# Kernel optimization log

Measured on AMD Instinct MI355X. Metric: run time of the kernel, lower is better.

The kernel has to match this reference:

```python
import jax, jax.numpy as jnp
import numpy as np

LAYER_NUMBER = 1  # coeff for query_key_layer_scaling; cancels mathematically
HEAD_DIM = 128

def setup_inputs() -> dict:
    key = jax.random.key(0)
    k1, k2, k3, k4 = jax.random.split(key, 4)
    s, b, h, d = 2048, 2, 16, HEAD_DIM
    return {
        "query_layer": jax.random.normal(k1, (s, b, h, d), dtype=jnp.float32),
        "key_layer": jax.random.normal(k2, (s, b, h, d), dtype=jnp.float32),
        "value_layer": jax.random.normal(k3, (s, b, h, d), dtype=jnp.float32),
        "attention_mask": jax.random.randint(k4, (b, 1, s, s), 0, 2).astype(jnp.bool_),
    }

def reference(query_layer, key_layer, value_layer, attention_mask):
    s, b, h, d = query_layer.shape
    # norm_factor = sqrt(d) * layer_number; softmax scale (coeff) = layer_number
    norm_factor = jnp.sqrt(jnp.asarray(d, jnp.float32)) * LAYER_NUMBER
    coeff = jnp.asarray(LAYER_NUMBER, jnp.float32)
    # raw scores [b, h, sq, sk]
    scores = jnp.einsum('sbhd,tbhd->bhst', query_layer, key_layer) / norm_factor
    # fused scale-mask-softmax, in fp32 (attention_softmax_in_fp32=True)
    scores32 = scores.astype(jnp.float32) * coeff
    scores32 = jnp.where(attention_mask, jnp.float32(-10000.0), scores32)
    probs = jax.nn.softmax(scores32, axis=-1).astype(query_layer.dtype)
    # dropout p=0.0 -> identity
    # context: [b, h, sq, d] -> [sq, b, h*d]
    ctx = jnp.einsum('bhst,tbhd->sbhd', probs, value_layer)
    return ctx.reshape(s, b, h * d)
```

## Files before the change

### kernel.cpp

```cpp
#include <hip/hip_runtime.h>
#include <hip/hip_bf16.h>

#define S_LEN 2048
#define NB 2
#define NH 16
#define DH 128
#define ROW_STRIDE (NB * NH * DH)
#define M_TILE 128
#define N_TILE 64
#define NKT (S_LEN / N_TILE)
#define NWORDS (NB * S_LEN * (S_LEN / 64))

typedef __bf16 bf16x8_t __attribute__((ext_vector_type(8)));
typedef __bf16 bf16x4_t __attribute__((ext_vector_type(4)));
typedef float  f32x4_t  __attribute__((ext_vector_type(4)));

#define AS1 __attribute__((address_space(1)))
#define AS3 __attribute__((address_space(3)))

__device__ __forceinline__ void gload_lds16(const void* g, void* l) {
    __builtin_amdgcn_global_load_lds((const AS1 void*)g, (AS3 void*)l, 16, 0, 0);
}

__device__ __forceinline__ float vexp2(float x) {
    float r;
    asm("v_exp_f32 %0, %1" : "=v"(r) : "v"(x));
    return r;
}
__device__ __forceinline__ unsigned vcvtpk(float a, float b) {
    unsigned r;
    asm("v_cvt_pk_bf16_f32 %0, %1, %2" : "=v"(r) : "v"(a), "v"(b));
    return r;
}

template <int CTRL>
__device__ __forceinline__ float dppmov(float x) {
    return __builtin_bit_cast(float,
        __builtin_amdgcn_update_dpp(0, __builtin_bit_cast(int, x), CTRL, 0xF, 0xF, true));
}
__device__ __forceinline__ float rowmax16(float x) {
    x = fmaxf(x, dppmov<0xB1>(x));
    x = fmaxf(x, dppmov<0x4E>(x));
    x = fmaxf(x, dppmov<0x141>(x));
    x = fmaxf(x, dppmov<0x140>(x));
    return x;
}
__device__ __forceinline__ float rowsum16(float x) {
    x += dppmov<0xB1>(x);
    x += dppmov<0x4E>(x);
    x += dppmov<0x141>(x);
    x += dppmov<0x140>(x);
    return x;
}

__global__ __launch_bounds__(256) void prep_kernel(
    const float* __restrict__ Kg, const float* __restrict__ Vg,
    const int* __restrict__ Mg,
    __bf16* __restrict__ Kb, __bf16* __restrict__ Vb,
    unsigned long long* __restrict__ Wg)
{
    __shared__ float tf[64][129];
    const int tid = threadIdx.x;
    const int blk = blockIdx.x;

    if (blk < 4096) {
        const int idx = blk * 256 + tid;
        const int d8 = (idx & 15) * 8;
        const int t  = (idx >> 4) & (S_LEN - 1);
        const int bh = idx >> 15;
        const int b = bh >> 4, h = bh & (NH - 1);
        const float* src = Kg + (size_t)t * ROW_STRIDE + b * (NH * DH) + h * DH + d8;
        float4 f0 = *(const float4*)src;
        float4 f1 = *(const float4*)(src + 4);
        bf16x8_t v;
        v[0] = (__bf16)f0.x; v[1] = (__bf16)f0.y; v[2] = (__bf16)f0.z; v[3] = (__bf16)f0.w;
        v[4] = (__bf16)f1.x; v[5] = (__bf16)f1.y; v[6] = (__bf16)f1.z; v[7] = (__bf16)f1.w;
        *(bf16x8_t*)(Kb + ((size_t)bh * S_LEN + t) * DH + d8) = v;
    } else if (blk < 5120) {
        const int vb = blk - 4096;
        const int bh = vb >> 5;
        const int tc = vb & 31;
        const int b = bh >> 4, h = bh & (NH - 1);
        const int t0 = tc * 64;
        const int head_off = b * (NH * DH) + h * DH;
#pragma unroll
        for (int i = 0; i < 8; ++i) {
            int idx = i * 256 + tid;
            int t  = idx >> 5;
            int d4 = (idx & 31) * 4;
            float4 f = *(const float4*)(Vg + (size_t)(t0 + t) * ROW_STRIDE + head_off + d4);
            tf[t][d4 + 0] = f.x; tf[t][d4 + 1] = f.y;
            tf[t][d4 + 2] = f.z; tf[t][d4 + 3] = f.w;
        }
        __syncthreads();
#pragma unroll
        for (int i = 0; i < 8; ++i) {
            int idx = i * 256 + tid;
            int d  = idx >> 4;
            int t4 = (idx & 15) * 4;
            bf16x4_t w;
            w[0] = (__bf16)tf[t4 + 0][d];
            w[1] = (__bf16)tf[t4 + 1][d];
            w[2] = (__bf16)tf[t4 + 2][d];
            w[3] = (__bf16)tf[t4 + 3][d];
            *(bf16x4_t*)(Vb + ((size_t)bh * DH + d) * S_LEN + t0 + t4) = w;
        }
    } else {
        const int lane = tid & 63;
        const int wv = ((blk - 5120) * 256 + tid) >> 6;
#pragma unroll
        for (int i = 0; i < 16; ++i) {
            const int wid = wv * 16 + i;
            const int v = Mg[(size_t)wid * 64 + lane];
            const unsigned long long bal = __ballot(v != 0);
            if (lane == 0) Wg[wid] = bal;
        }
    }
}

__global__ __launch_bounds__(256) void mask_pack(
    const int* __restrict__ Mg, unsigned long long* __restrict__ Wg)
{
    const int lane = threadIdx.x & 63;
    const int wv = (blockIdx.x * blockDim.x + threadIdx.x) >> 6;
#pragma unroll
    for (int i = 0; i < 4; ++i) {
        const int wid = wv * 4 + i;
        const int v = Mg[(size_t)wid * 64 + lane];
        const unsigned long long bal = __ballot(v != 0);
        if (lane == 0) Wg[wid] = bal;
    }
}

__global__ __launch_bounds__(256, 2) void fa_kernel(
    const float* __restrict__ Qg, const __bf16* __restrict__ Kb,
    const __bf16* __restrict__ Vb, const unsigned long long* __restrict__ Mw,
    float* __restrict__ Og)
{
    __shared__ __bf16 kT[2][64 * 128];
    __shared__ __bf16 vT[2][128 * 64];

    const int tid  = threadIdx.x;
    const int wave = tid >> 6;
    const int lane = tid & 63;
    const int l15  = lane & 15;
    const int quad = lane >> 4;
    const int swz  = (l15 & 7) << 4;

    const int bid = blockIdx.x;
    const int lb  = ((bid & 7) << 6) | (bid >> 3);
    const int qt  = lb & 15;
    const int bh  = lb >> 4;
    const int h   = bh & (NH - 1);
    const int b   = bh >> 4;

    const int q0       = qt * M_TILE;
    const int head_off = b * (NH * DH) + h * DH;

    const float kScale = 1.44269504088896340736f / 11.31370849898476039f;

    const uint2* mrow = (const uint2*)Mw
        + (size_t)b * (S_LEN * (S_LEN / 64))
        + (size_t)(q0 + wave * 32) * (S_LEN / 64);

    const char* KbBH = (const char*)(Kb + (size_t)bh * S_LEN * DH);
    const char* VbBH = (const char*)(Vb + (size_t)bh * DH * S_LEN);

    int kOff[4], vOff[4];
#pragma unroll
    for (int i = 0; i < 4; ++i) {
        const int chunk = (wave * 4 + i) * 64 + lane;
        const int tr = chunk >> 4;
        const int ck = chunk & 15;
        kOff[i] = tr * 256 + ((ck * 16) ^ ((tr & 7) << 4));
        const int dv = chunk >> 3;
        const int cv = chunk & 7;
        vOff[i] = dv * (S_LEN * 2) + ((cv * 16) ^ ((dv & 7) << 4));
    }

    bf16x8_t qf[2][4];
#pragma unroll
    for (int mt = 0; mt < 2; ++mt) {
        const int srow = q0 + wave * 32 + mt * 16 + l15;
        const float* qp = Qg + (size_t)srow * ROW_STRIDE + head_off + quad * 8;
#pragma unroll
        for (int kc = 0; kc < 4; ++kc) {
            float4 f0 = *(const float4*)(qp + kc * 32);
            float4 f1 = *(const float4*)(qp + kc * 32 + 4);
            bf16x8_t v;
            v[0] = (__bf16)(f0.x * kScale); v[1] = (__bf16)(f0.y * kScale);
            v[2] = (__bf16)(f0.z * kScale); v[3] = (__bf16)(f0.w * kScale);
            v[4] = (__bf16)(f1.x * kScale); v[5] = (__bf16)(f1.y * kScale);
            v[6] = (__bf16)(f1.z * kScale); v[7] = (__bf16)(f1.w * kScale);
            qf[mt][kc] = v;
        }
    }

    f32x4_t oacc[2][8];
    float lsum[2];
#pragma unroll
    for (int mt = 0; mt < 2; ++mt) {
#pragma unroll
        for (int dt = 0; dt < 8; ++dt) oacc[mt][dt] = {0.0f, 0.0f, 0.0f, 0.0f};
        lsum[mt] = 0.0f;
    }

    auto STAGE = [&](int buf, int kt_) {
        const char* ks = KbBH + (size_t)kt_ * (N_TILE * DH * 2);
        const char* vs = VbBH + (size_t)kt_ * (N_TILE * 2);
#pragma unroll
        for (int i = 0; i < 4; ++i)
            gload_lds16(ks + kOff[i], (char*)&kT[buf][0] + (wave * 4 + i) * 1024);
#pragma unroll
        for (int i = 0; i < 4; ++i)
            gload_lds16(vs + vOff[i], (char*)&vT[buf][0] + (wave * 4 + i) * 1024);
    };

    STAGE(0, 0);
    asm volatile("s_waitcnt vmcnt(0)" ::: "memory");
    __builtin_amdgcn_s_barrier();
    int cur = 0;

    for (int kt = 0; kt < NKT; ++kt) {
        if (kt + 1 < NKT) STAGE(cur ^ 1, kt + 1);

        uint2 mwv[2];
#pragma unroll
        for (int mt = 0; mt < 2; ++mt)
            mwv[mt] = mrow[(size_t)(mt * 16 + l15) * (S_LEN / 64) + kt];

        const char* kbuf = (const char*)&kT[cur][0];
        f32x4_t sacc[2][4];
#pragma unroll
        for (int mt = 0; mt < 2; ++mt)
#pragma unroll
            for (int n = 0; n < 4; ++n) sacc[mt][n] = {0.0f, 0.0f, 0.0f, 0.0f};
        __builtin_amdgcn_s_setprio(1);
#pragma unroll
        for (int n = 0; n < 4; ++n) {
#pragma unroll
            for (int kc = 0; kc < 4; ++kc) {
                bf16x8_t kb = *(const bf16x8_t*)(kbuf + (n * 16 + l15) * 256
                                                 + ((kc * 64 + quad * 16) ^ swz));
                sacc[0][n] = __builtin_amdgcn_mfma_f32_16x16x32_bf16(kb, qf[0][kc], sacc[0][n], 0, 0, 0);
                sacc[1][n] = __builtin_amdgcn_mfma_f32_16x16x32_bf16(kb, qf[1][kc], sacc[1][n], 0, 0, 0);
            }
        }
        __builtin_amdgcn_s_setprio(0);

        unsigned pk[2][4][2];
#pragma unroll
        for (int mt = 0; mt < 2; ++mt) {
            const unsigned ex0 = mwv[mt].x >> (quad * 4);
            const unsigned ex1 = mwv[mt].y >> (quad * 4);
            float p[4][4];
#pragma unroll
            for (int n = 0; n < 4; ++n) {
                const unsigned ex = (n < 2) ? ex0 : ex1;
                const int sh = (n & 1) * 16;
#pragma unroll
                for (int r = 0; r < 4; ++r) {
                    const float e = vexp2(sacc[mt][n][r]);
                    p[n][r] = ((ex >> (sh + r)) & 1u) ? 0.0f : e;
                }
            }
            float s01 = (p[0][0] + p[0][1]) + (p[0][2] + p[0][3]);
            float s11 = (p[1][0] + p[1][1]) + (p[1][2] + p[1][3]);
            float s21 = (p[2][0] + p[2][1]) + (p[2][2] + p[2][3]);
            float s31 = (p[3][0] + p[3][1]) + (p[3][2] + p[3][3]);
            lsum[mt] += (s01 + s11) + (s21 + s31);
#pragma unroll
            for (int n = 0; n < 4; ++n) {
                pk[mt][n][0] = vcvtpk(p[n][0], p[n][1]);
                pk[mt][n][1] = vcvtpk(p[n][2], p[n][3]);
            }
        }

        const char* vbuf = (const char*)&vT[cur][0];
        __builtin_amdgcn_s_setprio(1);
#pragma unroll
        for (int kc2 = 0; kc2 < 2; ++kc2) {
            bf16x8_t af[2];
#pragma unroll
            for (int mt = 0; mt < 2; ++mt) {
                int4 a;
                a.x = (int)pk[mt][2 * kc2][0];
                a.y = (int)pk[mt][2 * kc2][1];
                a.z = (int)pk[mt][2 * kc2 + 1][0];
                a.w = (int)pk[mt][2 * kc2 + 1][1];
                af[mt] = __builtin_bit_cast(bf16x8_t, a);
            }
#pragma unroll
            for (int dt = 0; dt < 8; ++dt) {
                const char* vrow = vbuf + (dt * 16 + l15) * 128;
                bf16x4_t v0 = *(const bf16x4_t*)(vrow + ((kc2 * 64 + quad * 8) ^ swz));
                bf16x4_t v1 = *(const bf16x4_t*)(vrow + ((kc2 * 64 + quad * 8 + 32) ^ swz));
                bf16x8_t bfr = __builtin_shufflevector(v0, v1, 0, 1, 2, 3, 4, 5, 6, 7);
                oacc[0][dt] = __builtin_amdgcn_mfma_f32_16x16x32_bf16(af[0], bfr, oacc[0][dt], 0, 0, 0);
                oacc[1][dt] = __builtin_amdgcn_mfma_f32_16x16x32_bf16(af[1], bfr, oacc[1][dt], 0, 0, 0);
            }
        }
        __builtin_amdgcn_s_setprio(0);

        asm volatile("s_waitcnt vmcnt(0)" ::: "memory");
        __builtin_amdgcn_s_barrier();
        cur ^= 1;
    }

#pragma unroll
    for (int mt = 0; mt < 2; ++mt) {
        float tot = lsum[mt];
        tot += __shfl_xor(tot, 16, 64);
        tot += __shfl_xor(tot, 32, 64);
#pragma unroll
        for (int r = 0; r < 4; ++r) {
            const float inv = 1.0f / __shfl(tot, quad * 4 + r, 64);
            const int srow = q0 + wave * 32 + mt * 16 + quad * 4 + r;
            float* op = Og + (size_t)srow * ROW_STRIDE + head_off + l15;
#pragma unroll
            for (int dt = 0; dt < 8; ++dt) op[dt * 16] = oacc[mt][dt][r] * inv;
        }
    }
}

#define LDS_KS 136
#define LDS_VS 72
#define LDS_PS 68

__global__ __launch_bounds__(256, 2) void fa_kernel_fb(
    const float* __restrict__ Qg, const float* __restrict__ Kg,
    const float* __restrict__ Vg, const unsigned long long* __restrict__ Mw,
    float* __restrict__ Og)
{
    __shared__ __bf16 kT[64 * LDS_KS];
    __shared__ __bf16 vT[DH * LDS_VS];
    __shared__ __bf16 pT[4 * 32 * LDS_PS];

    const int tid  = threadIdx.x;
    const int wave = tid >> 6;
    const int lane = tid & 63;
    const int l15  = lane & 15;
    const int quad = lane >> 4;

    const int bid = blockIdx.x;
    const int qt  = bid & 15;
    const int bh  = bid >> 4;
    const int h   = bh & (NH - 1);
    const int b   = bh >> 4;

    const int q0       = qt * M_TILE;
    const int head_off = b * (NH * DH) + h * DH;

    const float kScale   = 1.44269504088896340736f / 11.31370849898476039f;
    const float kMaskVal = -14426.950408889634f;
    const float kThr     = 8.0f;

    const uint2* mrow = (const uint2*)Mw
        + (size_t)b * (S_LEN * (S_LEN / 64))
        + (size_t)(q0 + wave * 32) * (S_LEN / 64);

    bf16x8_t qf[2][4];
#pragma unroll
    for (int mt = 0; mt < 2; ++mt) {
        const int srow = q0 + wave * 32 + mt * 16 + l15;
        const float* qp = Qg + (size_t)srow * ROW_STRIDE + head_off + quad * 8;
#pragma unroll
        for (int kc = 0; kc < 4; ++kc) {
            float4 f0 = *(const float4*)(qp + kc * 32);
            float4 f1 = *(const float4*)(qp + kc * 32 + 4);
            bf16x8_t v;
            v[0] = (__bf16)f0.x; v[1] = (__bf16)f0.y;
            v[2] = (__bf16)f0.z; v[3] = (__bf16)f0.w;
            v[4] = (__bf16)f1.x; v[5] = (__bf16)f1.y;
            v[6] = (__bf16)f1.z; v[7] = (__bf16)f1.w;
            qf[mt][kc] = v;
        }
    }

    f32x4_t oacc[2][8];
    float mstate[2][4], lstate[2][4];
#pragma unroll
    for (int mt = 0; mt < 2; ++mt) {
#pragma unroll
        for (int dt = 0; dt < 8; ++dt) oacc[mt][dt] = {0.0f, 0.0f, 0.0f, 0.0f};
#pragma unroll
        for (int r = 0; r < 4; ++r) { mstate[mt][r] = -3.0e38f; lstate[mt][r] = 0.0f; }
    }

    __bf16* pW = &pT[wave * 32 * LDS_PS];

    for (int kt = 0; kt < NKT; ++kt) {
        const int t0 = kt * N_TILE;
        __syncthreads();

        {
            const int r0 = tid >> 5;
            const int c4 = (tid & 31) * 4;
            const float* kp = Kg + (size_t)(t0 + r0) * ROW_STRIDE + head_off + c4;
            __bf16* kd = &kT[r0 * LDS_KS + c4];
#pragma unroll
            for (int rr = 0; rr < 8; ++rr) {
                float4 f = *(const float4*)kp;
                bf16x4_t w;
                w[0] = (__bf16)f.x; w[1] = (__bf16)f.y;
                w[2] = (__bf16)f.z; w[3] = (__bf16)f.w;
                *(bf16x4_t*)kd = w;
                kp += 8 * ROW_STRIDE;
                kd += 8 * LDS_KS;
            }
        }
        {
            const int dv = tid & 31;
            const int tg = tid >> 5;
            const float* vbase = Vg + (size_t)(t0 + tg * 8) * ROW_STRIDE + head_off + dv;
#pragma unroll
            for (int j = 0; j < 4; ++j) {
                const int d = dv + j * 32;
#pragma unroll
                for (int tt = 0; tt < 2; ++tt) {
                    const float* vp = vbase + j * 32 + (size_t)(tt * 4) * ROW_STRIDE;
                    bf16x4_t w;
                    w[0] = (__bf16)vp[0 * ROW_STRIDE];
                    w[1] = (__bf16)vp[1 * ROW_STRIDE];
                    w[2] = (__bf16)vp[2 * ROW_STRIDE];
                    w[3] = (__bf16)vp[3 * ROW_STRIDE];
                    *(bf16x4_t*)&vT[d * LDS_VS + tg * 8 + tt * 4] = w;
                }
            }
        }
        __syncthreads();

        uint2 mw[2][4];
#pragma unroll
        for (int mt = 0; mt < 2; ++mt)
#pragma unroll
            for (int r = 0; r < 4; ++r)
                mw[mt][r] = mrow[(size_t)(mt * 16 + quad * 4 + r) * (S_LEN / 64) + kt];

        f32x4_t sacc[2][4];
#pragma unroll
        for (int mt = 0; mt < 2; ++mt)
#pragma unroll
            for (int n = 0; n < 4; ++n) sacc[mt][n] = {0.0f, 0.0f, 0.0f, 0.0f};
#pragma unroll
        for (int n = 0; n < 4; ++n) {
#pragma unroll
            for (int kc = 0; kc < 4; ++kc) {
                bf16x8_t kb = *(const bf16x8_t*)&kT[(n * 16 + l15) * LDS_KS + kc * 32 + quad * 8];
                sacc[0][n] = __builtin_amdgcn_mfma_f32_16x16x32_bf16(qf[0][kc], kb, sacc[0][n], 0, 0, 0);
                sacc[1][n] = __builtin_amdgcn_mfma_f32_16x16x32_bf16(qf[1][kc], kb, sacc[1][n], 0, 0, 0);
            }
        }

#pragma unroll
        for (int mt = 0; mt < 2; ++mt) {
            float sv[4][4];
            float tmv[4];
#pragma unroll
            for (int r = 0; r < 4; ++r) {
                const unsigned a0 = mw[mt][r].x >> l15;
                const unsigned a1 = mw[mt][r].y >> l15;
                sv[0][r] = (a0 & 1u)       ? kMaskVal : sacc[mt][0][r] * kScale;
                sv[1][r] = (a0 & 0x10000u) ? kMaskVal : sacc[mt][1][r] * kScale;
                sv[2][r] = (a1 & 1u)       ? kMaskVal : sacc[mt][2][r] * kScale;
                sv[3][r] = (a1 & 0x10000u) ? kMaskVal : sacc[mt][3][r] * kScale;
                float tm = fmaxf(fmaxf(sv[0][r], sv[1][r]), fmaxf(sv[2][r], sv[3][r]));
                tmv[r] = rowmax16(tm);
            }
            bool need = (tmv[0] > mstate[mt][0] + kThr) |
                        (tmv[1] > mstate[mt][1] + kThr) |
                        (tmv[2] > mstate[mt][2] + kThr) |
                        (tmv[3] > mstate[mt][3] + kThr);
            if (__any(need)) {
#pragma unroll
                for (int r = 0; r < 4; ++r) {
                    const float mold  = mstate[mt][r];
                    const float mnew  = fmaxf(mold, tmv[r]);
                    const float alpha = vexp2(mold - mnew);
                    float rsum = 0.0f;
#pragma unroll
                    for (int n = 0; n < 4; ++n) {
                        float p = vexp2(sv[n][r] - mnew);
                        rsum += p;
                        pW[(mt * 16 + quad * 4 + r) * LDS_PS + n * 16 + l15] = (__bf16)p;
                    }
                    rsum = rowsum16(rsum);
                    lstate[mt][r] = lstate[mt][r] * alpha + rsum;
                    mstate[mt][r] = mnew;
#pragma unroll
                    for (int dt = 0; dt < 8; ++dt) oacc[mt][dt][r] *= alpha;
                }
            } else {
#pragma unroll
                for (int r = 0; r < 4; ++r) {
                    const float mold = mstate[mt][r];
                    float rsum = 0.0f;
#pragma unroll
                    for (int n = 0; n < 4; ++n) {
                        float p = vexp2(sv[n][r] - mold);
                        rsum += p;
                        pW[(mt * 16 + quad * 4 + r) * LDS_PS + n * 16 + l15] = (__bf16)p;
                    }
                    lstate[mt][r] += rowsum16(rsum);
                }
            }
        }

#pragma unroll
        for (int kc2 = 0; kc2 < 2; ++kc2) {
            bf16x8_t af[2];
#pragma unroll
            for (int mt = 0; mt < 2; ++mt) {
                bf16x4_t lo = *(const bf16x4_t*)&pW[(mt * 16 + l15) * LDS_PS + kc2 * 32 + quad * 8];
                bf16x4_t hi = *(const bf16x4_t*)&pW[(mt * 16 + l15) * LDS_PS + kc2 * 32 + quad * 8 + 4];
                af[mt] = __builtin_shufflevector(lo, hi, 0, 1, 2, 3, 4, 5, 6, 7);
            }
#pragma unroll
            for (int dt = 0; dt < 8; ++dt) {
                bf16x8_t bfr = *(const bf16x8_t*)&vT[(dt * 16 + l15) * LDS_VS + kc2 * 32 + quad * 8];
                oacc[0][dt] = __builtin_amdgcn_mfma_f32_16x16x32_bf16(af[0], bfr, oacc[0][dt], 0, 0, 0);
                oacc[1][dt] = __builtin_amdgcn_mfma_f32_16x16x32_bf16(af[1], bfr, oacc[1][dt], 0, 0, 0);
            }
        }
    }

#pragma unroll
    for (int mt = 0; mt < 2; ++mt) {
#pragma unroll
        for (int r = 0; r < 4; ++r) {
            const float inv = 1.0f / lstate[mt][r];
            const int srow = q0 + wave * 32 + mt * 16 + quad * 4 + r;
            float* op = Og + (size_t)srow * ROW_STRIDE + head_off + l15;
#pragma unroll
            for (int dt = 0; dt < 8; ++dt) op[dt * 16] = oacc[mt][dt][r] * inv;
        }
    }
}

extern "C" void kernel_launch(void* const* d_in, const int* in_sizes, int n_in,
                              void* d_out, int out_size, void* d_ws, size_t ws_size,
                              hipStream_t stream) {
    (void)in_sizes; (void)n_in; (void)out_size;
    const float* Q = (const float*)d_in[0];
    const float* K = (const float*)d_in[1];
    const float* V = (const float*)d_in[2];
    const int*   M = (const int*)d_in[3];
    float* O = (float*)d_out;

    const size_t need_fast = ((size_t)33 << 20);

    if (ws_size >= need_fast) {
        __bf16* Kb = (__bf16*)d_ws;
        __bf16* Vb = (__bf16*)((char*)d_ws + ((size_t)16 << 20));
        unsigned long long* Mw = (unsigned long long*)((char*)d_ws + ((size_t)32 << 20));
        hipLaunchKernelGGL(prep_kernel, dim3(7168), dim3(256), 0, stream, K, V, M, Kb, Vb, Mw);
        hipLaunchKernelGGL(fa_kernel, dim3(NB * NH * (S_LEN / M_TILE)), dim3(256), 0, stream,
                           Q, Kb, Vb, Mw, O);
    } else {
        unsigned long long* Mw = (unsigned long long*)d_ws;
        hipLaunchKernelGGL(mask_pack, dim3(NWORDS / 4 * 64 / 256), dim3(256), 0, stream, M, Mw);
        hipLaunchKernelGGL(fa_kernel_fb, dim3(NB * NH * (S_LEN / M_TILE)), dim3(256), 0, stream,
                           Q, K, V, Mw, O);
    }
}
```

Baseline: 259.7 us.

## Pre-swizzle K/V tiles in prep and use 8 waves of 16 query rows

The prep kernel now writes K and V as contiguous pre-swizzled 16KB bf16 tiles in exactly the LDS layout, so the attention kernel stages each tile with plain linear global-to-LDS copies and reads V fragments as single 16-byte loads instead of two 8-byte loads. The attention kernel moves from 4 waves handling 32 query rows each to 8 waves (512 threads) handling 16 rows each, halving per-wave accumulator registers to raise occupancy. The trade-off is fewer MFMAs per K/V LDS fragment load, since each K and V fragment now feeds one query tile instead of two, which raises LDS traffic per unit of work.

```diff
diff --git a/kernel.cpp b/kernel.cpp
--- a/kernel.cpp
+++ b/kernel.cpp
@@ -63,32 +63,38 @@
     const int tid = threadIdx.x;
     const int blk = blockIdx.x;
 
-    if (blk < 4096) {
-        const int idx = blk * 256 + tid;
-        const int d8 = (idx & 15) * 8;
-        const int t  = (idx >> 4) & (S_LEN - 1);
-        const int bh = idx >> 15;
+    if (blk < 1024) {
+        const int bh = blk >> 5;
+        const int kt = blk & 31;
         const int b = bh >> 4, h = bh & (NH - 1);
-        const float* src = Kg + (size_t)t * ROW_STRIDE + b * (NH * DH) + h * DH + d8;
-        float4 f0 = *(const float4*)src;
-        float4 f1 = *(const float4*)(src + 4);
-        bf16x8_t v;
-        v[0] = (__bf16)f0.x; v[1] = (__bf16)f0.y; v[2] = (__bf16)f0.z; v[3] = (__bf16)f0.w;
-        v[4] = (__bf16)f1.x; v[5] = (__bf16)f1.y; v[6] = (__bf16)f1.z; v[7] = (__bf16)f1.w;
-        *(bf16x8_t*)(Kb + ((size_t)bh * S_LEN + t) * DH + d8) = v;
-    } else if (blk < 5120) {
-        const int vb = blk - 4096;
+        const int head_off = b * (NH * DH) + h * DH;
+        char* tile = (char*)Kb + (size_t)blk * 16384;
+#pragma unroll
+        for (int it = 0; it < 4; ++it) {
+            const int idx = it * 256 + tid;
+            const int tl = idx >> 4;
+            const int d8 = (idx & 15) * 8;
+            const float* src = Kg + (size_t)(kt * 64 + tl) * ROW_STRIDE + head_off + d8;
+            float4 f0 = *(const float4*)src;
+            float4 f1 = *(const float4*)(src + 4);
+            bf16x8_t v;
+            v[0] = (__bf16)f0.x; v[1] = (__bf16)f0.y; v[2] = (__bf16)f0.z; v[3] = (__bf16)f0.w;
+            v[4] = (__bf16)f1.x; v[5] = (__bf16)f1.y; v[6] = (__bf16)f1.z; v[7] = (__bf16)f1.w;
+            *(bf16x8_t*)(tile + tl * 256 + ((d8 * 2) ^ ((tl & 7) << 4))) = v;
+        }
+    } else if (blk < 2048) {
+        const int vb = blk - 1024;
         const int bh = vb >> 5;
-        const int tc = vb & 31;
+        const int kt = vb & 31;
         const int b = bh >> 4, h = bh & (NH - 1);
-        const int t0 = tc * 64;
         const int head_off = b * (NH * DH) + h * DH;
+        char* tile = (char*)Vb + (size_t)vb * 16384;
 #pragma unroll
         for (int i = 0; i < 8; ++i) {
             int idx = i * 256 + tid;
             int t  = idx >> 5;
             int d4 = (idx & 31) * 4;
-            float4 f = *(const float4*)(Vg + (size_t)(t0 + t) * ROW_STRIDE + head_off + d4);
+            float4 f = *(const float4*)(Vg + (size_t)(kt * 64 + t) * ROW_STRIDE + head_off + d4);
             tf[t][d4 + 0] = f.x; tf[t][d4 + 1] = f.y;
             tf[t][d4 + 2] = f.z; tf[t][d4 + 3] = f.w;
         }
@@ -103,11 +109,12 @@
             w[1] = (__bf16)tf[t4 + 1][d];
             w[2] = (__bf16)tf[t4 + 2][d];
             w[3] = (__bf16)tf[t4 + 3][d];
-            *(bf16x4_t*)(Vb + ((size_t)bh * DH + d) * S_LEN + t0 + t4) = w;
+            const int col = (t4 & 32) * 2 + ((t4 >> 2) & 3) * 16 + ((t4 & 16) >> 1);
+            *(bf16x4_t*)(tile + d * 128 + (col ^ ((d & 7) << 4))) = w;
         }
     } else {
         const int lane = tid & 63;
-        const int wv = ((blk - 5120) * 256 + tid) >> 6;
+        const int wv = ((blk - 2048) * 256 + tid) >> 6;
 #pragma unroll
         for (int i = 0; i < 16; ++i) {
             const int wid = wv * 16 + i;
@@ -132,7 +139,7 @@
     }
 }
 
-__global__ __launch_bounds__(256, 2) void fa_kernel(
+__global__ __launch_bounds__(512, 4) void fa_kernel(
     const float* __restrict__ Qg, const __bf16* __restrict__ Kb,
     const __bf16* __restrict__ Vb, const unsigned long long* __restrict__ Mw,
     float* __restrict__ Og)
@@ -161,27 +168,14 @@
 
     const uint2* mrow = (const uint2*)Mw
         + (size_t)b * (S_LEN * (S_LEN / 64))
-        + (size_t)(q0 + wave * 32) * (S_LEN / 64);
-
-    const char* KbBH = (const char*)(Kb + (size_t)bh * S_LEN * DH);
-    const char* VbBH = (const char*)(Vb + (size_t)bh * DH * S_LEN);
-
-    int kOff[4], vOff[4];
-#pragma unroll
-    for (int i = 0; i < 4; ++i) {
-        const int chunk = (wave * 4 + i) * 64 + lane;
-        const int tr = chunk >> 4;
-        const int ck = chunk & 15;
-        kOff[i] = tr * 256 + ((ck * 16) ^ ((tr & 7) << 4));
-        const int dv = chunk >> 3;
-        const int cv = chunk & 7;
-        vOff[i] = dv * (S_LEN * 2) + ((cv * 16) ^ ((dv & 7) << 4));
-    }
-
-    bf16x8_t qf[2][4];
-#pragma unroll
-    for (int mt = 0; mt < 2; ++mt) {
-        const int srow = q0 + wave * 32 + mt * 16 + l15;
+        + (size_t)(q0 + wave * 16) * (S_LEN / 64);
+
+    const char* KbBH = (const char*)Kb + (size_t)bh * (NKT * 16384);
+    const char* VbBH = (const char*)Vb + (size_t)bh * (NKT * 16384);
+
+    bf16x8_t qf[4];
+    {
+        const int srow = q0 + wave * 16 + l15;
         const float* qp = Qg + (size_t)srow * ROW_STRIDE + head_off + quad * 8;
 #pragma unroll
         for (int kc = 0; kc < 4; ++kc) {
@@ -192,28 +186,24 @@
             v[2] = (__bf16)(f0.z * kScale); v[3] = (__bf16)(f0.w * kScale);
             v[4] = (__bf16)(f1.x * kScale); v[5] = (__bf16)(f1.y * kScale);
             v[6] = (__bf16)(f1.z * kScale); v[7] = (__bf16)(f1.w * kScale);
-            qf[mt][kc] = v;
-        }
-    }
-
-    f32x4_t oacc[2][8];
-    float lsum[2];
-#pragma unroll
-    for (int mt = 0; mt < 2; ++mt) {
-#pragma unroll
-        for (int dt = 0; dt < 8; ++dt) oacc[mt][dt] = {0.0f, 0.0f, 0.0f, 0.0f};
-        lsum[mt] = 0.0f;
-    }
+            qf[kc] = v;
+        }
+    }
+
+    f32x4_t oacc[8];
+    float lsum = 0.0f;
+#pragma unroll
+    for (int dt = 0; dt < 8; ++dt) oacc[dt] = {0.0f, 0.0f, 0.0f, 0.0f};
 
     auto STAGE = [&](int buf, int kt_) {
-        const char* ks = KbBH + (size_t)kt_ * (N_TILE * DH * 2);
-        const char* vs = VbBH + (size_t)kt_ * (N_TILE * 2);
-#pragma unroll
-        for (int i = 0; i < 4; ++i)
-            gload_lds16(ks + kOff[i], (char*)&kT[buf][0] + (wave * 4 + i) * 1024);
-#pragma unroll
-        for (int i = 0; i < 4; ++i)
-            gload_lds16(vs + vOff[i], (char*)&vT[buf][0] + (wave * 4 + i) * 1024);
+        const char* ks = KbBH + (size_t)kt_ * 16384;
+        const char* vs = VbBH + (size_t)kt_ * 16384;
+#pragma unroll
+        for (int i = 0; i < 2; ++i) {
+            const int c = (wave * 2 + i) * 1024;
+            gload_lds16(ks + c + lane * 16, (char*)&kT[buf][0] + c);
+            gload_lds16(vs + c + lane * 16, (char*)&vT[buf][0] + c);
+        }
     };
 
     STAGE(0, 0);
@@ -224,17 +214,12 @@
     for (int kt = 0; kt < NKT; ++kt) {
         if (kt + 1 < NKT) STAGE(cur ^ 1, kt + 1);
 
-        uint2 mwv[2];
-#pragma unroll
-        for (int mt = 0; mt < 2; ++mt)
-            mwv[mt] = mrow[(size_t)(mt * 16 + l15) * (S_LEN / 64) + kt];
+        const uint2 mwv = mrow[(size_t)l15 * (S_LEN / 64) + kt];
 
         const char* kbuf = (const char*)&kT[cur][0];
-        f32x4_t sacc[2][4];
-#pragma unroll
-        for (int mt = 0; mt < 2; ++mt)
-#pragma unroll
-            for (int n = 0; n < 4; ++n) sacc[mt][n] = {0.0f, 0.0f, 0.0f, 0.0f};
+        f32x4_t sacc[4];
+#pragma unroll
+        for (int n = 0; n < 4; ++n) sacc[n] = {0.0f, 0.0f, 0.0f, 0.0f};
         __builtin_amdgcn_s_setprio(1);
 #pragma unroll
         for (int n = 0; n < 4; ++n) {
@@ -242,17 +227,15 @@
             for (int kc = 0; kc < 4; ++kc) {
                 bf16x8_t kb = *(const bf16x8_t*)(kbuf + (n * 16 + l15) * 256
                                                  + ((kc * 64 + quad * 16) ^ swz));
-                sacc[0][n] = __builtin_amdgcn_mfma_f32_16x16x32_bf16(kb, qf[0][kc], sacc[0][n], 0, 0, 0);
-                sacc[1][n] = __builtin_amdgcn_mfma_f32_16x16x32_bf16(kb, qf[1][kc], sacc[1][n], 0, 0, 0);
+                sacc[n] = __builtin_amdgcn_mfma_f32_16x16x32_bf16(kb, qf[kc], sacc[n], 0, 0, 0);
             }
         }
         __builtin_amdgcn_s_setprio(0);
 
-        unsigned pk[2][4][2];
-#pragma unroll
-        for (int mt = 0; mt < 2; ++mt) {
-            const unsigned ex0 = mwv[mt].x >> (quad * 4);
-            const unsigned ex1 = mwv[mt].y >> (quad * 4);
+        unsigned pk[4][2];
+        {
+            const unsigned ex0 = mwv.x >> (quad * 4);
+            const unsigned ex1 = mwv.y >> (quad * 4);
             float p[4][4];
 #pragma unroll
             for (int n = 0; n < 4; ++n) {
@@ -260,19 +243,19 @@
                 const int sh = (n & 1) * 16;
 #pragma unroll
                 for (int r = 0; r < 4; ++r) {
-                    const float e = vexp2(sacc[mt][n][r]);
+                    const float e = vexp2(sacc[n][r]);
                     p[n][r] = ((ex >> (sh + r)) & 1u) ? 0.0f : e;
                 }
             }
-            float s01 = (p[0][0] + p[0][1]) + (p[0][2] + p[0][3]);
-            float s11 = (p[1][0] + p[1][1]) + (p[1][2] + p[1][3]);
-            float s21 = (p[2][0] + p[2][1]) + (p[2][2] + p[2][3]);
-            float s31 = (p[3][0] + p[3][1]) + (p[3][2] + p[3][3]);
-            lsum[mt] += (s01 + s11) + (s21 + s31);
+            float s0 = (p[0][0] + p[0][1]) + (p[0][2] + p[0][3]);
+            float s1 = (p[1][0] + p[1][1]) + (p[1][2] + p[1][3]);
+            float s2 = (p[2][0] + p[2][1]) + (p[2][2] + p[2][3]);
+            float s3 = (p[3][0] + p[3][1]) + (p[3][2] + p[3][3]);
+            lsum += (s0 + s1) + (s2 + s3);
 #pragma unroll
             for (int n = 0; n < 4; ++n) {
-                pk[mt][n][0] = vcvtpk(p[n][0], p[n][1]);
-                pk[mt][n][1] = vcvtpk(p[n][2], p[n][3]);
+                pk[n][0] = vcvtpk(p[n][0], p[n][1]);
+                pk[n][1] = vcvtpk(p[n][2], p[n][3]);
             }
         }
 
@@ -280,24 +263,17 @@
         __builtin_amdgcn_s_setprio(1);
 #pragma unroll
         for (int kc2 = 0; kc2 < 2; ++kc2) {
-            bf16x8_t af[2];
-#pragma unroll
-            for (int mt = 0; mt < 2; ++mt) {
-                int4 a;
-                a.x = (int)pk[mt][2 * kc2][0];
-                a.y = (int)pk[mt][2 * kc2][1];
-                a.z = (int)pk[mt][2 * kc2 + 1][0];
-                a.w = (int)pk[mt][2 * kc2 + 1][1];
-                af[mt] = __builtin_bit_cast(bf16x8_t, a);
-            }
+            int4 a;
+            a.x = (int)pk[2 * kc2][0];
+            a.y = (int)pk[2 * kc2][1];
+            a.z = (int)pk[2 * kc2 + 1][0];
+            a.w = (int)pk[2 * kc2 + 1][1];
+            const bf16x8_t af = __builtin_bit_cast(bf16x8_t, a);
 #pragma unroll
             for (int dt = 0; dt < 8; ++dt) {
-                const char* vrow = vbuf + (dt * 16 + l15) * 128;
-                bf16x4_t v0 = *(const bf16x4_t*)(vrow + ((kc2 * 64 + quad * 8) ^ swz));
-                bf16x4_t v1 = *(const bf16x4_t*)(vrow + ((kc2 * 64 + quad * 8 + 32) ^ swz));
-                bf16x8_t bfr = __builtin_shufflevector(v0, v1, 0, 1, 2, 3, 4, 5, 6, 7);
-                oacc[0][dt] = __builtin_amdgcn_mfma_f32_16x16x32_bf16(af[0], bfr, oacc[0][dt], 0, 0, 0);
-                oacc[1][dt] = __builtin_amdgcn_mfma_f32_16x16x32_bf16(af[1], bfr, oacc[1][dt], 0, 0, 0);
+                bf16x8_t bfr = *(const bf16x8_t*)(vbuf + (dt * 16 + l15) * 128
+                                                  + ((kc2 * 64 + quad * 16) ^ swz));
+                oacc[dt] = __builtin_amdgcn_mfma_f32_16x16x32_bf16(af, bfr, oacc[dt], 0, 0, 0);
             }
         }
         __builtin_amdgcn_s_setprio(0);
@@ -307,19 +283,16 @@
         cur ^= 1;
     }
 
-#pragma unroll
-    for (int mt = 0; mt < 2; ++mt) {
-        float tot = lsum[mt];
-        tot += __shfl_xor(tot, 16, 64);
-        tot += __shfl_xor(tot, 32, 64);
-#pragma unroll
-        for (int r = 0; r < 4; ++r) {
-            const float inv = 1.0f / __shfl(tot, quad * 4 + r, 64);
-            const int srow = q0 + wave * 32 + mt * 16 + quad * 4 + r;
-            float* op = Og + (size_t)srow * ROW_STRIDE + head_off + l15;
-#pragma unroll
-            for (int dt = 0; dt < 8; ++dt) op[dt * 16] = oacc[mt][dt][r] * inv;
-        }
+    float tot = lsum;
+    tot += __shfl_xor(tot, 16, 64);
+    tot += __shfl_xor(tot, 32, 64);
+#pragma unroll
+    for (int r = 0; r < 4; ++r) {
+        const float inv = 1.0f / __shfl(tot, quad * 4 + r, 64);
+        const int srow = q0 + wave * 16 + quad * 4 + r;
+        float* op = Og + (size_t)srow * ROW_STRIDE + head_off + l15;
+#pragma unroll
+        for (int dt = 0; dt < 8; ++dt) op[dt * 16] = oacc[dt][r] * inv;
     }
 }
 
@@ -553,8 +526,8 @@
         __bf16* Kb = (__bf16*)d_ws;
         __bf16* Vb = (__bf16*)((char*)d_ws + ((size_t)16 << 20));
         unsigned long long* Mw = (unsigned long long*)((char*)d_ws + ((size_t)32 << 20));
-        hipLaunchKernelGGL(prep_kernel, dim3(7168), dim3(256), 0, stream, K, V, M, Kb, Vb, Mw);
-        hipLaunchKernelGGL(fa_kernel, dim3(NB * NH * (S_LEN / M_TILE)), dim3(256), 0, stream,
+        hipLaunchKernelGGL(prep_kernel, dim3(4096), dim3(256), 0, stream, K, V, M, Kb, Vb, Mw);
+        hipLaunchKernelGGL(fa_kernel, dim3(NB * NH * (S_LEN / M_TILE)), dim3(512), 0, stream,
                            Q, Kb, Vb, Mw, O);
     } else {
         unsigned long long* Mw = (unsigned long long*)d_ws;
```

Result: faster. 247.5 us (-4.7%).
